# Kernel optimization log

Hardware: AMD Instinct MI355X
Metric: run time of the kernel (lower is better)

Reference implementation:

```python
import jax, jax.numpy as jnp
import numpy as np

SIGMA = 1.0
SQRT2 = float(np.sqrt(2.0))


def setup_inputs() -> dict:
    key = jax.random.key(0)
    k1, k2 = jax.random.split(key)
    B, L = 128, 1024
    preds = jax.random.normal(k1, (B, L), dtype=jnp.float32)
    # integer relevance grades 0..4, stored as float as in the torch module
    target = jax.random.randint(k2, (B, L), 0, 5).astype(jnp.float32)
    return {"preds": preds, "target": target}


def reference(preds, target):
    B, L = preds.shape
    # pairwise diff [B, L, L]: diff[b,i,j] = preds[b,i] - preds[b,j]
    diff = preds[:, :, None] - preds[:, None, :]
    # Normal(0, sigma*sqrt(2)).cdf(diff) == ndtr(diff / (sigma*sqrt(2)))
    p = jax.scipy.special.ndtr(diff / (SIGMA * SQRT2))
    # zero the diagonal (i == j) before summing
    eye = jnp.eye(L, dtype=bool)
    p = jnp.where(eye[None, :, :], 0.0, p)
    expected_ranks = 1.0 + p.sum(axis=2)  # [B, L]

    gains = 2.0 ** target - 1.0
    discounts = jnp.log2(expected_ranks + 1.0)
    dcg = (gains / discounts).sum(axis=1)  # [B]

    ideal_target = jnp.sort(target, axis=1)[:, ::-1]  # descending
    ideal_gains = 2.0 ** ideal_target - 1.0
    ideal_discounts = jnp.log2(jnp.arange(1, L + 1, dtype=jnp.float32) + 1.0)
    idcg = (ideal_gains / ideal_discounts).sum(axis=1)  # [B]

    ndcg = dcg / (idcg + 1e-10)
    return -ndcg.mean()
```

## Files before the change

### kernel.cpp

```cpp
#include <hip/hip_runtime.h>

#define B 128
#define L 1024

#if __has_builtin(__builtin_amdgcn_exp2f)
#define EXP2(x) __builtin_amdgcn_exp2f(x)
#else
#define EXP2(x) __expf((x) * 0.6931471805599453f)
#endif

#define WS_ACC  1048576
#define WS_GCTR 1048577

#define K1 -1.6279072f
#define K2 -0.9299637f
#define K3 -0.1074808f

__device__ __forceinline__ float ror16(float x) {
    int i = __float_as_int(x);
    i = __builtin_amdgcn_update_dpp(i, i, 0x121 , 0xF, 0xF, true);
    return __int_as_float(i);
}

__global__ __launch_bounds__(256, 8) void pair_kernel(const float* __restrict__ preds,
                                                      float* __restrict__ ws) {
    __shared__ float sp[L];
    __shared__ float ebuf[L];

    const int blk  = blockIdx.x;
    const int b    = blk >> 3;
    const int hb   = blk & 7;
    const int tid  = threadIdx.x;
    const int l16  = tid & 15;
    const int ring = tid >> 4;
    const int slot = hb * 16 + ring;
    const int g    = slot & 63;
    const int half = slot >> 6;

    if (blk == 0 && tid == 0) {
        ws[WS_ACC] = 0.0f;
        ((int*)ws)[WS_GCTR] = 0;
    }

    const float* prow = preds + b * L;
    float4 v = reinterpret_cast<const float4*>(prow)[tid];
    v.x *= 0.5f; v.y *= 0.5f; v.z *= 0.5f; v.w *= 0.5f;
    reinterpret_cast<float4*>(sp)[tid] = v;
    reinterpret_cast<float4*>(ebuf)[tid] = make_float4(0.f, 0.f, 0.f, 0.f);
    __syncthreads();

    const float pi = sp[g * 16 + l16];
    float Ei = 0.0f;

    const int nt = half ? (16 + (g < 32 ? 1 : 0)) : 16;
    for (int si = 0; si < nt; ++si) {
        const int s  = half ? (16 + si) : si;
        const int gj = (g + s) & 63;
        float pj = sp[gj * 16 + l16];
        float ej = 0.0f;
        #pragma unroll
        for (int k = 0; k < 16; ++k) {
            pj = ror16(pj);
            float d = pi - pj;
            float a = __builtin_fabsf(d);
            float t = __builtin_fmaf(K3, a, K2);
            float u = __builtin_fmaf(t, a, K1);
            float e = EXP2(a * u);
            float r = __builtin_copysignf(1.0f - e, d);
            Ei += r;
            ej = ror16(ej) - r;
        }
        if (s != 0)
            atomicAdd(&ebuf[gj * 16 + l16], ej);
    }
    atomicAdd(&ebuf[g * 16 + l16], Ei);
    __syncthreads();

    float4 r4 = reinterpret_cast<float4*>(ebuf)[tid];
    reinterpret_cast<float4*>(ws + (size_t)blk * L)[tid] = r4;
}

__global__ __launch_bounds__(256) void finish_kernel(const float* __restrict__ target,
                                                     float* __restrict__ ws,
                                                     float* __restrict__ out) {
    __shared__ unsigned long long cred[256];
    __shared__ float2 fred[256];

    const int b   = blockIdx.x;
    const int tid = threadIdx.x;
    const float* trow = target + b * L;

    float dcg_p = 0.0f;
    unsigned long long cnt = 0ull;
    #pragma unroll
    for (int k = 0; k < 4; ++k) {
        const int i = tid + k * 256;
        float E = 0.0f;
        #pragma unroll
        for (int hb = 0; hb < 8; ++hb)
            E += ws[(size_t)(b * 8 + hb) * L + i];
        float er1 = 513.5f + 0.5f * E;
        float t = trow[i];
        dcg_p += (EXP2(t) - 1.0f) * __builtin_amdgcn_rcpf(__log2f(er1));
        cnt += ((unsigned long long)(t > 3.5f) << 48)
             + ((unsigned long long)(t > 2.5f) << 32)
             + ((unsigned long long)(t > 1.5f) << 16)
             + ((unsigned long long)(t > 0.5f));
    }
    cred[tid] = cnt;
    __syncthreads();
    #pragma unroll
    for (int s = 128; s > 0; s >>= 1) {
        if (tid < (unsigned)s) cred[tid] += cred[tid + s];
        __syncthreads();
    }
    const unsigned long long tot = cred[0];
    const int n4 = (int)(tot >> 48) & 0xFFFF;
    const int n3 = (int)(tot >> 32) & 0xFFFF;
    const int n2 = (int)(tot >> 16) & 0xFFFF;
    const int n1 = (int)(tot)       & 0xFFFF;

    float idcg_p = 0.0f;
    #pragma unroll
    for (int k = 0; k < 4; ++k) {
        int pos = tid + 1 + k * 256;
        float gain = (pos <= n4) ? 15.0f : (pos <= n3) ? 7.0f :
                     (pos <= n2) ? 3.0f  : (pos <= n1) ? 1.0f : 0.0f;
        idcg_p += gain * __builtin_amdgcn_rcpf(__log2f((float)pos + 1.0f));
    }
    fred[tid] = make_float2(idcg_p, dcg_p);
    __syncthreads();
    #pragma unroll
    for (int s = 128; s > 0; s >>= 1) {
        if (tid < (unsigned)s) {
            float2 x = fred[tid], y = fred[tid + s];
            fred[tid] = make_float2(x.x + y.x, x.y + y.y);
        }
        __syncthreads();
    }

    if (tid == 0) {
        float ndcg = fred[0].y / (fred[0].x + 1e-10f);
        atomicAdd(&ws[WS_ACC], ndcg);
        __threadfence();
        int old = atomicAdd((int*)ws + WS_GCTR, 1);
        if (old == B - 1) {
            float acc = atomicAdd(&ws[WS_ACC], 0.0f);
            out[0] = -acc * (1.0f / (float)B);
        }
    }
}

extern "C" void kernel_launch(void* const* d_in, const int* in_sizes, int n_in,
                              void* d_out, int out_size, void* d_ws, size_t ws_size,
                              hipStream_t stream) {
    const float* preds  = (const float*)d_in[0];
    const float* target = (const float*)d_in[1];
    float* out = (float*)d_out;
    float* ws  = (float*)d_ws;

    pair_kernel<<<B * 8, 256, 0, stream>>>(preds, ws);
    finish_kernel<<<B, 256, 0, stream>>>(target, ws, out);
}
```

Before: 88.96 us.

## Split pair work across 16 blocks per row and interleave two tile streams

Each batch row now gets 16 blocks instead of 8. Every block handles 8 shift offsets for a quarter of the groups, and one pair of blocks takes the extra shift-32 tile. The inner loop processes two neighbour tiles at once to expose instruction-level parallelism across the exp/FMA chains. The intent is more grid parallelism, so the GPU's CUs are better filled, and better latency hiding. In exchange the workspace partials double and the finish kernel does twice as many reads.

```diff
diff --git a/kernel.cpp b/kernel.cpp
--- a/kernel.cpp
+++ b/kernel.cpp
@@ -9,8 +9,8 @@
 #define EXP2(x) __expf((x) * 0.6931471805599453f)
 #endif
 
-#define WS_ACC  1048576
-#define WS_GCTR 1048577
+#define WS_ACC  2097152
+#define WS_GCTR 2097153
 
 #define K1 -1.6279072f
 #define K2 -0.9299637f
@@ -28,14 +28,14 @@
     __shared__ float ebuf[L];
 
     const int blk  = blockIdx.x;
-    const int b    = blk >> 3;
-    const int hb   = blk & 7;
+    const int b    = blk >> 4;
+    const int qb   = blk & 15;
     const int tid  = threadIdx.x;
     const int l16  = tid & 15;
     const int ring = tid >> 4;
-    const int slot = hb * 16 + ring;
-    const int g    = slot & 63;
-    const int half = slot >> 6;
+    const int g    = (qb & 3) * 16 + ring;
+    const int base_s = (qb >> 2) * 8;
+    const bool has32 = ((qb >> 1) == 6);
 
     if (blk == 0 && tid == 0) {
         ws[WS_ACC] = 0.0f;
@@ -50,12 +50,36 @@
     __syncthreads();
 
     const float pi = sp[g * 16 + l16];
-    float Ei = 0.0f;
+    float Ei1 = 0.0f, Ei2 = 0.0f;
 
-    const int nt = half ? (16 + (g < 32 ? 1 : 0)) : 16;
-    for (int si = 0; si < nt; ++si) {
-        const int s  = half ? (16 + si) : si;
-        const int gj = (g + s) & 63;
+    for (int s = base_s; s < base_s + 8; s += 2) {
+        const int gj1 = (g + s) & 63;
+        const int gj2 = (g + s + 1) & 63;
+        float pj1 = sp[gj1 * 16 + l16];
+        float pj2 = sp[gj2 * 16 + l16];
+        float ej1 = 0.0f, ej2 = 0.0f;
+        #pragma unroll
+        for (int k = 0; k < 16; ++k) {
+            pj1 = ror16(pj1);
+            pj2 = ror16(pj2);
+            float d1 = pi - pj1,                  d2 = pi - pj2;
+            float a1 = __builtin_fabsf(d1),       a2 = __builtin_fabsf(d2);
+            float t1 = __builtin_fmaf(K3, a1, K2), t2 = __builtin_fmaf(K3, a2, K2);
+            float u1 = __builtin_fmaf(t1, a1, K1), u2 = __builtin_fmaf(t2, a2, K1);
+            float e1 = EXP2(a1 * u1),             e2 = EXP2(a2 * u2);
+            float r1 = __builtin_copysignf(1.0f - e1, d1);
+            float r2 = __builtin_copysignf(1.0f - e2, d2);
+            Ei1 += r1;                            Ei2 += r2;
+            ej1 = ror16(ej1) - r1;
+            ej2 = ror16(ej2) - r2;
+        }
+        if (s != 0)
+            atomicAdd(&ebuf[gj1 * 16 + l16], ej1);
+        atomicAdd(&ebuf[gj2 * 16 + l16], ej2);
+    }
+
+    if (has32) {
+        const int gj = (g + 32) & 63;
         float pj = sp[gj * 16 + l16];
         float ej = 0.0f;
         #pragma unroll
@@ -67,13 +91,13 @@
             float u = __builtin_fmaf(t, a, K1);
             float e = EXP2(a * u);
             float r = __builtin_copysignf(1.0f - e, d);
-            Ei += r;
+            Ei1 += r;
             ej = ror16(ej) - r;
         }
-        if (s != 0)
-            atomicAdd(&ebuf[gj * 16 + l16], ej);
+        atomicAdd(&ebuf[gj * 16 + l16], ej);
     }
-    atomicAdd(&ebuf[g * 16 + l16], Ei);
+
+    atomicAdd(&ebuf[g * 16 + l16], Ei1 + Ei2);
     __syncthreads();
 
     float4 r4 = reinterpret_cast<float4*>(ebuf)[tid];
@@ -97,8 +121,8 @@
         const int i = tid + k * 256;
         float E = 0.0f;
         #pragma unroll
-        for (int hb = 0; hb < 8; ++hb)
-            E += ws[(size_t)(b * 8 + hb) * L + i];
+        for (int qb = 0; qb < 16; ++qb)
+            E += ws[(size_t)(b * 16 + qb) * L + i];
         float er1 = 513.5f + 0.5f * E;
         float t = trow[i];
         dcg_p += (EXP2(t) - 1.0f) * __builtin_amdgcn_rcpf(__log2f(er1));
@@ -159,6 +183,6 @@
     float* out = (float*)d_out;
     float* ws  = (float*)d_ws;
 
-    pair_kernel<<<B * 8, 256, 0, stream>>>(preds, ws);
+    pair_kernel<<<B * 16, 256, 0, stream>>>(preds, ws);
     finish_kernel<<<B, 256, 0, stream>>>(target, ws, out);
 }
```

New measurement: 93.03 us. +4.6%, slower.
